# Performance work log

Hardware: AMD Instinct MI355X
Metric: run time of the kernel (lower is better)

Reference implementation:

```python
import jax, jax.numpy as jnp
import numpy as np

DIM = 256
NUM_HEADS = 8


def setup_inputs() -> dict:
    key = jax.random.key(0)
    ks = jax.random.split(key, 8)
    B, H, W = 2, 64, 64
    s = 0.02
    return {
        "query": jax.random.normal(ks[0], (B, H, W, DIM), jnp.float32),
        "sim": jax.random.normal(ks[1], (B, H, W, DIM), jnp.float32),
        "Wq": jax.random.normal(ks[2], (DIM, DIM), jnp.float32) * s,
        "bq": jnp.zeros((DIM,), jnp.float32),
        "Wkv": jax.random.normal(ks[3], (DIM, 2 * DIM), jnp.float32) * s,
        "bkv": jnp.zeros((2 * DIM,), jnp.float32),
        "Wp": jax.random.normal(ks[4], (DIM, DIM), jnp.float32) * s,
        "bp": jnp.zeros((DIM,), jnp.float32),
    }


def reference(query, sim, Wq, bq, Wkv, bkv, Wp, bp):
    B, H, W, dim = query.shape
    nh = NUM_HEADS
    dh = dim // nh
    scale = dh ** (-0.5)
    S = H * W

    # projections
    q = (query.reshape(B, S, dim) @ Wq + bq).reshape(B, S, nh, dh)
    kv = (sim.reshape(B, S, dim) @ Wkv + bkv).reshape(B, S, 2, nh, dh)
    k = kv[:, :, 0]  # [B,S,nh,dh]
    v = kv[:, :, 1]

    # attention: scores [B,nh,S,S]
    attn = jnp.einsum('bqhd,bkhd->bhqk', q * scale, k)
    attn = jax.nn.softmax(attn, axis=-1)
    x = jnp.einsum('bhqk,bkhd->bqhd', attn, v)  # [B,S,nh,dh]
    x = x.reshape(B, H, W, dim)
    return x @ Wp + bp
```

## Files before the change

kernel.cpp:

```cpp
#include <hip/hip_runtime.h>
#include <hip/hip_bf16.h>
#include <math.h>


#define SCALE 0.17677669529663687f
#define LOG2E 1.4426950408889634f

typedef __attribute__((ext_vector_type(8))) short short8;
typedef __attribute__((ext_vector_type(8))) _Float16 half8;
typedef __attribute__((ext_vector_type(4))) float f32x4;

static __device__ __forceinline__ unsigned short f2bf(float x) {
    union { float f; unsigned int u; } v; v.f = x;
    unsigned int r = v.u + 0x7fff + ((v.u >> 16) & 1);
    return (unsigned short)(r >> 16);
}
static __device__ __forceinline__ float bf2f(unsigned short h) {
    union { unsigned int u; float f; } v; v.u = ((unsigned int)h) << 16;
    return v.f;
}
static __device__ __forceinline__ float fexp2(float x) {
#if __has_builtin(__builtin_amdgcn_exp2f)
    return __builtin_amdgcn_exp2f(x);
#else
    float r; asm("v_exp_f32 %0, %1" : "=v"(r) : "v"(x)); return r;
#endif
}
static __device__ __forceinline__ unsigned int pk_bf16(float a, float b) {
    unsigned int r;
    asm("v_cvt_pk_bf16_f32 %0, %1, %2" : "=v"(r) : "v"(a), "v"(b));
    return r;
}
static __device__ __forceinline__ unsigned short f2h(float x) {
    _Float16 h = (_Float16)x;
    union { _Float16 h; unsigned short s; } u; u.h = h;
    return u.s;
}
static __device__ __forceinline__ float h2f(unsigned short s) {
    union { _Float16 h; unsigned short s; } u; u.s = s;
    return (float)u.h;
}

__global__ __launch_bounds__(256) void prep(
    const float* __restrict__ query, const float* __restrict__ sim,
    const float* __restrict__ Wq, const float* __restrict__ Wkv,
    const float* __restrict__ Wp,
    unsigned short* __restrict__ xhi, unsigned short* __restrict__ xlo,
    unsigned short* __restrict__ wfp)
{
    __shared__ float T[64][68];
    const int blk = blockIdx.x, t = threadIdx.x;
    if (blk < 4096) {
        const int e = blk * 1024 + t * 4;
        const float* src = (e < 2097152) ? (query + e) : (sim + (e - 2097152));
        float4 v = *(const float4*)src;
        float xv[4] = {v.x, v.y, v.z, v.w};
        union { unsigned short s[4]; uint2 u; } ph, pl;
#pragma unroll
        for (int j = 0; j < 4; ++j) {
            unsigned short h = f2h(xv[j]);
            ph.s[j] = h;
            pl.s[j] = f2h(xv[j] - h2f(h));
        }
        *(uint2*)&xhi[e] = ph.u;
        *(uint2*)&xlo[e] = pl.u;
        return;
    }
    const int bb = blk - 4096;
    const int mat = bb >> 4, tile = bb & 15;
    const int kr0 = (tile >> 2) * 64;
    const int nc0 = (tile & 3) * 64;
    const float* src; int ldw, cb; float sc = 1.f;
    if (mat == 0)      { src = Wq;  ldw = 256; cb = 0;   sc = SCALE * LOG2E; }
    else if (mat == 1) { src = Wkv; ldw = 512; cb = 0;   }
    else if (mat == 2) { src = Wkv; ldw = 512; cb = 256; }
    else               { src = Wp;  ldw = 256; cb = 0;   }
    {
        const int rl = t >> 4, c4 = (t & 15) * 4;
#pragma unroll
        for (int rr = 0; rr < 4; ++rr) {
            float4 v = *(const float4*)&src[(long long)(kr0 + rr * 16 + rl) * ldw + cb + nc0 + c4];
            T[rr * 16 + rl][c4 + 0] = v.x; T[rr * 16 + rl][c4 + 1] = v.y;
            T[rr * 16 + rl][c4 + 2] = v.z; T[rr * 16 + rl][c4 + 3] = v.w;
        }
    }
    __syncthreads();
    {
        const int nl = t >> 2, kl0 = (t & 3) * 16;
        const long long orow = (long long)(mat * 256 + nc0 + nl) * 256 + kr0 + kl0;
        union { unsigned short s[16]; uint4 u[2]; } ph;
#pragma unroll
        for (int j = 0; j < 16; ++j)
            ph.s[j] = f2h(T[kl0 + j][nl] * sc);
        *(uint4*)&wfp[orow] = ph.u[0];
        *(uint4*)&wfp[orow + 8] = ph.u[1];
    }
}

__global__ __launch_bounds__(256) void gemm_qkv(
    const unsigned short* __restrict__ xhi, const unsigned short* __restrict__ xlo,
    const unsigned short* __restrict__ wfp,
    const float* __restrict__ bq, const float* __restrict__ bkv,
    unsigned short* __restrict__ qbuf, unsigned short* __restrict__ kbuf,
    unsigned short* __restrict__ vTb)
{
    __shared__ unsigned short XsH[64 * 40], XsL[64 * 40], Ws[64 * 40];

    const int t = threadIdx.x, wave = t >> 6, lane = t & 63;
    const int col = lane & 15, quad = lane >> 4;
    const int by = blockIdx.y;
    const int kind = by >> 2;
    const int n0 = (by & 3) * 64;
    const int m0 = blockIdx.x * 64;
    const int xrow0 = ((kind == 0) ? 0 : 8192) + m0;
    const int wrow0 = kind * 256 + n0;
    const int srow = t >> 2, spart = (t & 3) * 8;

    const f32x4 zero = {0.f, 0.f, 0.f, 0.f};
    f32x4 acc[4] = {zero, zero, zero, zero};

    for (int kt = 0; kt < 8; ++kt) {
        const int k0 = kt * 32;
        uint4 xh = *(const uint4*)&xhi[(long long)(xrow0 + srow) * 256 + k0 + spart];
        uint4 xl = *(const uint4*)&xlo[(long long)(xrow0 + srow) * 256 + k0 + spart];
        uint4 wh = *(const uint4*)&wfp[(long long)(wrow0 + srow) * 256 + k0 + spart];
        __syncthreads();
        *(uint4*)&XsH[srow * 40 + spart] = xh;
        *(uint4*)&XsL[srow * 40 + spart] = xl;
        *(uint4*)&Ws[srow * 40 + spart] = wh;
        __syncthreads();

        if (kind < 2) {
            half8 a_h = *(const half8*)(XsH + (wave * 16 + col) * 40 + quad * 8);
            half8 a_l = *(const half8*)(XsL + (wave * 16 + col) * 40 + quad * 8);
#pragma unroll
            for (int nt = 0; nt < 4; ++nt) {
                half8 b = *(const half8*)(Ws + (nt * 16 + col) * 40 + quad * 8);
                acc[nt] = __builtin_amdgcn_mfma_f32_16x16x32_f16(a_h, b, acc[nt], 0, 0, 0);
                acc[nt] = __builtin_amdgcn_mfma_f32_16x16x32_f16(a_l, b, acc[nt], 0, 0, 0);
            }
        } else {
            half8 a = *(const half8*)(Ws + (wave * 16 + col) * 40 + quad * 8);
#pragma unroll
            for (int nt = 0; nt < 4; ++nt) {
                half8 b_h = *(const half8*)(XsH + (nt * 16 + col) * 40 + quad * 8);
                half8 b_l = *(const half8*)(XsL + (nt * 16 + col) * 40 + quad * 8);
                acc[nt] = __builtin_amdgcn_mfma_f32_16x16x32_f16(a, b_h, acc[nt], 0, 0, 0);
                acc[nt] = __builtin_amdgcn_mfma_f32_16x16x32_f16(a, b_l, acc[nt], 0, 0, 0);
            }
        }
    }

    if (kind == 0) {
#pragma unroll
        for (int nt = 0; nt < 4; ++nt) {
            int n = n0 + nt * 16 + col;
            int h = n >> 5, d = n & 31;
            float bias = bq[n] * (SCALE * LOG2E);
#pragma unroll
            for (int r = 0; r < 4; ++r) {
                int mg = m0 + wave * 16 + quad * 4 + r;
                int b = mg >> 12, sidx = mg & 4095;
                qbuf[((long long)(b * 8 + h) * 4096 + sidx) * 32 + d] = f2bf(acc[nt][r] + bias);
            }
        }
    } else if (kind == 1) {
#pragma unroll
        for (int nt = 0; nt < 4; ++nt) {
            int n = n0 + nt * 16 + col;
            int h = n >> 5, d = n & 31;
            float bias = bkv[n];
#pragma unroll
            for (int r = 0; r < 4; ++r) {
                int mg = m0 + wave * 16 + quad * 4 + r;
                int b = mg >> 12, sidx = mg & 4095;
                kbuf[((long long)(b * 8 + h) * 4096 + sidx) * 32 + d] = f2bf(acc[nt][r] + bias);
            }
        }
    } else {
#pragma unroll
        for (int nt = 0; nt < 4; ++nt) {
            int s = m0 + nt * 16 + col;
            int b = s >> 12, sidx = s & 4095;
#pragma unroll
            for (int r = 0; r < 4; ++r) {
                int dcol = n0 + wave * 16 + quad * 4 + r;
                int h = dcol >> 5, dd = dcol & 31;
                float bias = bkv[256 + dcol];
                vTb[((long long)((b * 8 + h) * 32 + dd)) * 4096 + sidx] = f2bf(acc[nt][r] + bias);
            }
        }
    }
}

__global__ __launch_bounds__(256) void flash_mfma(
    const unsigned short* __restrict__ qbuf,
    const unsigned short* __restrict__ kbuf,
    const unsigned short* __restrict__ vT,
    float* __restrict__ xbuf)
{
    __shared__ unsigned short Ks[128 * 40];
    __shared__ unsigned short Vt[32 * 136];
    __shared__ unsigned short Pb[4][640];

    const int t = threadIdx.x;
    const int wave = t >> 6, lane = t & 63;
    const int col = lane & 15, quad = lane >> 4;
    const int bh = blockIdx.x >> 5;
    const int q0 = (blockIdx.x & 31) * 128 + wave * 32;
    const long long kvbase = (long long)bh * 4096 * 32;
    unsigned short* pbw = Pb[wave];

    const short8 qf0 = *(const short8*)(qbuf + kvbase + (long long)(q0 + col) * 32 + quad * 8);
    const short8 qf1 = *(const short8*)(qbuf + kvbase + (long long)(q0 + 16 + col) * 32 + quad * 8);

    const f32x4 zero = {0.f, 0.f, 0.f, 0.f};
    f32x4 o00 = zero, o01 = zero, o10 = zero, o11 = zero;
    float l0 = 0.f, l1 = 0.f;

    const int krow = t >> 2, kpart = (t & 3) * 8;
    const int vrow = t >> 4, vpart = (t & 15) * 8;

    for (int kt = 0; kt < 32; ++kt) {
        uint4 kg0 = *(const uint4*)(kbuf + kvbase + (long long)(kt * 128 + krow) * 32 + kpart);
        uint4 kg1 = *(const uint4*)(kbuf + kvbase + (long long)(kt * 128 + krow + 64) * 32 + kpart);
        uint4 vg0 = *(const uint4*)(vT + ((long long)(bh * 32 + vrow)) * 4096 + kt * 128 + vpart);
        uint4 vg1 = *(const uint4*)(vT + ((long long)(bh * 32 + vrow + 16)) * 4096 + kt * 128 + vpart);
        __syncthreads();
        *(uint4*)(Ks + krow * 40 + kpart) = kg0;
        *(uint4*)(Ks + (krow + 64) * 40 + kpart) = kg1;
        *(uint4*)(Vt + vrow * 136 + vpart) = vg0;
        *(uint4*)(Vt + (vrow + 16) * 136 + vpart) = vg1;
        __syncthreads();

#pragma unroll
        for (int sb = 0; sb < 4; ++sb) {
            const int kb = sb * 32;
            short8 a0 = *(const short8*)(Ks + (kb + col) * 40 + quad * 8);
            short8 a1 = *(const short8*)(Ks + (kb + 16 + col) * 40 + quad * 8);
            short8 v0 = *(const short8*)(Vt + col * 136 + kb + quad * 8);
            short8 v1 = *(const short8*)(Vt + (16 + col) * 136 + kb + quad * 8);
            {
                f32x4 c0 = __builtin_amdgcn_mfma_f32_16x16x32_bf16(a0, qf0, zero, 0, 0, 0);
                f32x4 c1 = __builtin_amdgcn_mfma_f32_16x16x32_bf16(a1, qf0, zero, 0, 0, 0);
                float p0 = fexp2(c0[0]), p1 = fexp2(c0[1]), p2 = fexp2(c0[2]), p3 = fexp2(c0[3]);
                float p4 = fexp2(c1[0]), p5 = fexp2(c1[1]), p6 = fexp2(c1[2]), p7 = fexp2(c1[3]);
                l0 += ((p0 + p1) + (p2 + p3)) + ((p4 + p5) + (p6 + p7));
                uint2 w0 = make_uint2(pk_bf16(p0, p1), pk_bf16(p2, p3));
                uint2 w1 = make_uint2(pk_bf16(p4, p5), pk_bf16(p6, p7));
                *(uint2*)(pbw + col * 40 + quad * 4) = w0;
                *(uint2*)(pbw + col * 40 + 16 + quad * 4) = w1;
                short8 pf = *(const short8*)(pbw + col * 40 + quad * 8);
                o00 = __builtin_amdgcn_mfma_f32_16x16x32_bf16(v0, pf, o00, 0, 0, 0);
                o01 = __builtin_amdgcn_mfma_f32_16x16x32_bf16(v1, pf, o01, 0, 0, 0);
            }
            {
                f32x4 c0 = __builtin_amdgcn_mfma_f32_16x16x32_bf16(a0, qf1, zero, 0, 0, 0);
                f32x4 c1 = __builtin_amdgcn_mfma_f32_16x16x32_bf16(a1, qf1, zero, 0, 0, 0);
                float p0 = fexp2(c0[0]), p1 = fexp2(c0[1]), p2 = fexp2(c0[2]), p3 = fexp2(c0[3]);
                float p4 = fexp2(c1[0]), p5 = fexp2(c1[1]), p6 = fexp2(c1[2]), p7 = fexp2(c1[3]);
                l1 += ((p0 + p1) + (p2 + p3)) + ((p4 + p5) + (p6 + p7));
                uint2 w0 = make_uint2(pk_bf16(p0, p1), pk_bf16(p2, p3));
                uint2 w1 = make_uint2(pk_bf16(p4, p5), pk_bf16(p6, p7));
                *(uint2*)(pbw + col * 40 + quad * 4) = w0;
                *(uint2*)(pbw + col * 40 + 16 + quad * 4) = w1;
                short8 pf = *(const short8*)(pbw + col * 40 + quad * 8);
                o10 = __builtin_amdgcn_mfma_f32_16x16x32_bf16(v0, pf, o10, 0, 0, 0);
                o11 = __builtin_amdgcn_mfma_f32_16x16x32_bf16(v1, pf, o11, 0, 0, 0);
            }
        }
    }

    l0 += __shfl_xor(l0, 16, 64); l0 += __shfl_xor(l0, 32, 64);
    l1 += __shfl_xor(l1, 16, 64); l1 += __shfl_xor(l1, 32, 64);
    const float i0 = 1.f / l0, i1 = 1.f / l1;

    const int b = bh >> 3, hh = bh & 7;
    float* xp0 = xbuf + ((long long)(b * 4096 + q0 + col)) * 256 + hh * 32;
    *(float4*)(xp0 + quad * 4)      = make_float4(o00[0] * i0, o00[1] * i0, o00[2] * i0, o00[3] * i0);
    *(float4*)(xp0 + 16 + quad * 4) = make_float4(o01[0] * i0, o01[1] * i0, o01[2] * i0, o01[3] * i0);
    float* xp1 = xbuf + ((long long)(b * 4096 + q0 + 16 + col)) * 256 + hh * 32;
    *(float4*)(xp1 + quad * 4)      = make_float4(o10[0] * i1, o10[1] * i1, o10[2] * i1, o10[3] * i1);
    *(float4*)(xp1 + 16 + quad * 4) = make_float4(o11[0] * i1, o11[1] * i1, o11[2] * i1, o11[3] * i1);
}

__global__ __launch_bounds__(256) void gemm_outp(
    const float* __restrict__ xbuf, const unsigned short* __restrict__ wfp,
    const float* __restrict__ bp, float* __restrict__ out)
{
    __shared__ unsigned short XsH[64 * 40], XsL[64 * 40], Ws[64 * 40];

    const int t = threadIdx.x, wave = t >> 6, lane = t & 63;
    const int col = lane & 15, quad = lane >> 4;
    const int n0 = blockIdx.y * 64;
    const int m0 = blockIdx.x * 64;
    const int wrow0 = 768 + n0;
    const int srow = t >> 2, spart = (t & 3) * 8;

    const f32x4 zero = {0.f, 0.f, 0.f, 0.f};
    f32x4 acc[4] = {zero, zero, zero, zero};

    for (int kt = 0; kt < 8; ++kt) {
        const int k0 = kt * 32;
        const float* xp = &xbuf[(long long)(m0 + srow) * 256 + k0 + spart];
        float4 xa = *(const float4*)xp;
        float4 xb = *(const float4*)(xp + 4);
        float xv[8] = {xa.x, xa.y, xa.z, xa.w, xb.x, xb.y, xb.z, xb.w};
        union { unsigned short s[8]; uint4 u; } ph, pl;
#pragma unroll
        for (int j = 0; j < 8; ++j) {
            unsigned short h = f2h(xv[j]);
            ph.s[j] = h;
            pl.s[j] = f2h(xv[j] - h2f(h));
        }
        uint4 wh = *(const uint4*)&wfp[(long long)(wrow0 + srow) * 256 + k0 + spart];
        __syncthreads();
        *(uint4*)&XsH[srow * 40 + spart] = ph.u;
        *(uint4*)&XsL[srow * 40 + spart] = pl.u;
        *(uint4*)&Ws[srow * 40 + spart] = wh;
        __syncthreads();

        half8 a_h = *(const half8*)(XsH + (wave * 16 + col) * 40 + quad * 8);
        half8 a_l = *(const half8*)(XsL + (wave * 16 + col) * 40 + quad * 8);
#pragma unroll
        for (int nt = 0; nt < 4; ++nt) {
            half8 b = *(const half8*)(Ws + (nt * 16 + col) * 40 + quad * 8);
            acc[nt] = __builtin_amdgcn_mfma_f32_16x16x32_f16(a_h, b, acc[nt], 0, 0, 0);
            acc[nt] = __builtin_amdgcn_mfma_f32_16x16x32_f16(a_l, b, acc[nt], 0, 0, 0);
        }
    }

#pragma unroll
    for (int nt = 0; nt < 4; ++nt) {
        int n = n0 + nt * 16 + col;
        float bias = bp[n];
#pragma unroll
        for (int r = 0; r < 4; ++r) {
            int mg = m0 + wave * 16 + quad * 4 + r;
            out[(long long)mg * 256 + n] = acc[nt][r] + bias;
        }
    }
}

extern "C" void kernel_launch(void* const* d_in, const int* in_sizes, int n_in,
                              void* d_out, int out_size, void* d_ws, size_t ws_size,
                              hipStream_t stream) {
    const float* query = (const float*)d_in[0];
    const float* sim   = (const float*)d_in[1];
    const float* Wq    = (const float*)d_in[2];
    const float* bq    = (const float*)d_in[3];
    const float* Wkv   = (const float*)d_in[4];
    const float* bkv   = (const float*)d_in[5];
    const float* Wp    = (const float*)d_in[6];
    const float* bp    = (const float*)d_in[7];
    float* out = (float*)d_out;

    unsigned short* wsb = (unsigned short*)d_ws;
    unsigned short* qbuf = wsb;
    unsigned short* kbuf = wsb + 2097152;
    unsigned short* vT   = wsb + 4194304;
    unsigned short* wfp  = wsb + 6291456;
    unsigned short* xhi  = wsb + 6553600;
    unsigned short* xlo  = wsb + 10747904;
    float* xbuf = (float*)(wsb + 6553600);

    prep      <<<dim3(4160),    256, 0, stream>>>(query, sim, Wq, Wkv, Wp,
                                                  xhi, xlo, wfp);
    gemm_qkv  <<<dim3(128, 12), 256, 0, stream>>>(xhi, xlo, wfp, bq, bkv,
                                                  qbuf, kbuf, vT);
    flash_mfma<<<dim3(512),     256, 0, stream>>>(qbuf, kbuf, vT, xbuf);
    gemm_outp <<<dim3(128, 4),  256, 0, stream>>>(xbuf, wfp, bp, out);
}
```

Baseline: 172.6 us.

## Split attention KV range in two and raise queries per wave to four tiles

Each wave of the flash kernel now handles 64 queries instead of 32, so every K/V tile staged in shared memory feeds twice as much work. The key sequence is split into two halves across blocks to keep the grid size at 512. Each half writes unnormalized partial outputs and row sums, and the output projection combines the halves and normalizes them while loading. In exchange, the flash kernel uses more registers and shared memory, and the partial outputs double the traffic into the final GEMM. Dropping the running max relies on the score range being small, which the code before already assumed.

```diff
diff --git a/kernel.cpp b/kernel.cpp
--- a/kernel.cpp
+++ b/kernel.cpp
@@ -197,31 +197,35 @@
     const unsigned short* __restrict__ qbuf,
     const unsigned short* __restrict__ kbuf,
     const unsigned short* __restrict__ vT,
-    float* __restrict__ xbuf)
+    float* __restrict__ xpart, float* __restrict__ lpart)
 {
     __shared__ unsigned short Ks[128 * 40];
     __shared__ unsigned short Vt[32 * 136];
-    __shared__ unsigned short Pb[4][640];
+    __shared__ unsigned short Pb[16][640];
 
     const int t = threadIdx.x;
     const int wave = t >> 6, lane = t & 63;
     const int col = lane & 15, quad = lane >> 4;
-    const int bh = blockIdx.x >> 5;
-    const int q0 = (blockIdx.x & 31) * 128 + wave * 32;
+    const int qb = blockIdx.x & 15;
+    const int bh = (blockIdx.x >> 4) & 15;
+    const int ks = blockIdx.x >> 8;
+    const int q0 = qb * 256 + wave * 64;
     const long long kvbase = (long long)bh * 4096 * 32;
-    unsigned short* pbw = Pb[wave];
-
-    const short8 qf0 = *(const short8*)(qbuf + kvbase + (long long)(q0 + col) * 32 + quad * 8);
-    const short8 qf1 = *(const short8*)(qbuf + kvbase + (long long)(q0 + 16 + col) * 32 + quad * 8);
+
+    short8 qf[4];
+#pragma unroll
+    for (int i = 0; i < 4; ++i)
+        qf[i] = *(const short8*)(qbuf + kvbase + (long long)(q0 + i * 16 + col) * 32 + quad * 8);
 
     const f32x4 zero = {0.f, 0.f, 0.f, 0.f};
-    f32x4 o00 = zero, o01 = zero, o10 = zero, o11 = zero;
-    float l0 = 0.f, l1 = 0.f;
+    f32x4 o[8] = {zero, zero, zero, zero, zero, zero, zero, zero};
+    float l[4] = {0.f, 0.f, 0.f, 0.f};
 
     const int krow = t >> 2, kpart = (t & 3) * 8;
     const int vrow = t >> 4, vpart = (t & 15) * 8;
 
-    for (int kt = 0; kt < 32; ++kt) {
+    for (int kt0 = 0; kt0 < 16; ++kt0) {
+        const int kt = ks * 16 + kt0;
         uint4 kg0 = *(const uint4*)(kbuf + kvbase + (long long)(kt * 128 + krow) * 32 + kpart);
         uint4 kg1 = *(const uint4*)(kbuf + kvbase + (long long)(kt * 128 + krow + 64) * 32 + kpart);
         uint4 vg0 = *(const uint4*)(vT + ((long long)(bh * 32 + vrow)) * 4096 + kt * 128 + vpart);
@@ -240,52 +244,49 @@
             short8 a1 = *(const short8*)(Ks + (kb + 16 + col) * 40 + quad * 8);
             short8 v0 = *(const short8*)(Vt + col * 136 + kb + quad * 8);
             short8 v1 = *(const short8*)(Vt + (16 + col) * 136 + kb + quad * 8);
-            {
-                f32x4 c0 = __builtin_amdgcn_mfma_f32_16x16x32_bf16(a0, qf0, zero, 0, 0, 0);
-                f32x4 c1 = __builtin_amdgcn_mfma_f32_16x16x32_bf16(a1, qf0, zero, 0, 0, 0);
+#pragma unroll
+            for (int i = 0; i < 4; ++i) {
+                f32x4 c0 = __builtin_amdgcn_mfma_f32_16x16x32_bf16(a0, qf[i], zero, 0, 0, 0);
+                f32x4 c1 = __builtin_amdgcn_mfma_f32_16x16x32_bf16(a1, qf[i], zero, 0, 0, 0);
                 float p0 = fexp2(c0[0]), p1 = fexp2(c0[1]), p2 = fexp2(c0[2]), p3 = fexp2(c0[3]);
                 float p4 = fexp2(c1[0]), p5 = fexp2(c1[1]), p6 = fexp2(c1[2]), p7 = fexp2(c1[3]);
-                l0 += ((p0 + p1) + (p2 + p3)) + ((p4 + p5) + (p6 + p7));
+                l[i] += ((p0 + p1) + (p2 + p3)) + ((p4 + p5) + (p6 + p7));
                 uint2 w0 = make_uint2(pk_bf16(p0, p1), pk_bf16(p2, p3));
                 uint2 w1 = make_uint2(pk_bf16(p4, p5), pk_bf16(p6, p7));
+                unsigned short* pbw = Pb[wave * 4 + i];
                 *(uint2*)(pbw + col * 40 + quad * 4) = w0;
                 *(uint2*)(pbw + col * 40 + 16 + quad * 4) = w1;
                 short8 pf = *(const short8*)(pbw + col * 40 + quad * 8);
-                o00 = __builtin_amdgcn_mfma_f32_16x16x32_bf16(v0, pf, o00, 0, 0, 0);
-                o01 = __builtin_amdgcn_mfma_f32_16x16x32_bf16(v1, pf, o01, 0, 0, 0);
-            }
-            {
-                f32x4 c0 = __builtin_amdgcn_mfma_f32_16x16x32_bf16(a0, qf1, zero, 0, 0, 0);
-                f32x4 c1 = __builtin_amdgcn_mfma_f32_16x16x32_bf16(a1, qf1, zero, 0, 0, 0);
-                float p0 = fexp2(c0[0]), p1 = fexp2(c0[1]), p2 = fexp2(c0[2]), p3 = fexp2(c0[3]);
-                float p4 = fexp2(c1[0]), p5 = fexp2(c1[1]), p6 = fexp2(c1[2]), p7 = fexp2(c1[3]);
-                l1 += ((p0 + p1) + (p2 + p3)) + ((p4 + p5) + (p6 + p7));
-                uint2 w0 = make_uint2(pk_bf16(p0, p1), pk_bf16(p2, p3));
-                uint2 w1 = make_uint2(pk_bf16(p4, p5), pk_bf16(p6, p7));
-                *(uint2*)(pbw + col * 40 + quad * 4) = w0;
-                *(uint2*)(pbw + col * 40 + 16 + quad * 4) = w1;
-                short8 pf = *(const short8*)(pbw + col * 40 + quad * 8);
-                o10 = __builtin_amdgcn_mfma_f32_16x16x32_bf16(v0, pf, o10, 0, 0, 0);
-                o11 = __builtin_amdgcn_mfma_f32_16x16x32_bf16(v1, pf, o11, 0, 0, 0);
-            }
-        }
-    }
-
-    l0 += __shfl_xor(l0, 16, 64); l0 += __shfl_xor(l0, 32, 64);
-    l1 += __shfl_xor(l1, 16, 64); l1 += __shfl_xor(l1, 32, 64);
-    const float i0 = 1.f / l0, i1 = 1.f / l1;
+                o[2 * i]     = __builtin_amdgcn_mfma_f32_16x16x32_bf16(v0, pf, o[2 * i], 0, 0, 0);
+                o[2 * i + 1] = __builtin_amdgcn_mfma_f32_16x16x32_bf16(v1, pf, o[2 * i + 1], 0, 0, 0);
+            }
+        }
+    }
+
+#pragma unroll
+    for (int i = 0; i < 4; ++i) {
+        l[i] += __shfl_xor(l[i], 16, 64);
+        l[i] += __shfl_xor(l[i], 32, 64);
+    }
 
     const int b = bh >> 3, hh = bh & 7;
-    float* xp0 = xbuf + ((long long)(b * 4096 + q0 + col)) * 256 + hh * 32;
-    *(float4*)(xp0 + quad * 4)      = make_float4(o00[0] * i0, o00[1] * i0, o00[2] * i0, o00[3] * i0);
-    *(float4*)(xp0 + 16 + quad * 4) = make_float4(o01[0] * i0, o01[1] * i0, o01[2] * i0, o01[3] * i0);
-    float* xp1 = xbuf + ((long long)(b * 4096 + q0 + 16 + col)) * 256 + hh * 32;
-    *(float4*)(xp1 + quad * 4)      = make_float4(o10[0] * i1, o10[1] * i1, o10[2] * i1, o10[3] * i1);
-    *(float4*)(xp1 + 16 + quad * 4) = make_float4(o11[0] * i1, o11[1] * i1, o11[2] * i1, o11[3] * i1);
+    float* xp = xpart + (long long)ks * 2097152;
+#pragma unroll
+    for (int i = 0; i < 4; ++i) {
+        float* row = xp + ((long long)(b * 4096 + q0 + i * 16 + col)) * 256 + hh * 32;
+        *(float4*)(row + quad * 4)      = make_float4(o[2*i][0], o[2*i][1], o[2*i][2], o[2*i][3]);
+        *(float4*)(row + 16 + quad * 4) = make_float4(o[2*i+1][0], o[2*i+1][1], o[2*i+1][2], o[2*i+1][3]);
+    }
+    float lv = l[0];
+    if (quad == 1) lv = l[1];
+    else if (quad == 2) lv = l[2];
+    else if (quad == 3) lv = l[3];
+    lpart[ks * 65536 + bh * 4096 + q0 + quad * 16 + col] = lv;
 }
 
 __global__ __launch_bounds__(256) void gemm_outp(
-    const float* __restrict__ xbuf, const unsigned short* __restrict__ wfp,
+    const float* __restrict__ xpart, const float* __restrict__ lpart,
+    const unsigned short* __restrict__ wfp,
     const float* __restrict__ bp, float* __restrict__ out)
 {
     __shared__ unsigned short XsH[64 * 40], XsL[64 * 40], Ws[64 * 40];
@@ -296,22 +297,34 @@
     const int m0 = blockIdx.x * 64;
     const int wrow0 = 768 + n0;
     const int srow = t >> 2, spart = (t & 3) * 8;
+    const int r = m0 + srow;
+    const int bidx = r >> 12, s = r & 4095;
+    const float* __restrict__ xa = xpart;
+    const float* __restrict__ xb = xpart + 2097152;
 
     const f32x4 zero = {0.f, 0.f, 0.f, 0.f};
     f32x4 acc[4] = {zero, zero, zero, zero};
 
     for (int kt = 0; kt < 8; ++kt) {
         const int k0 = kt * 32;
-        const float* xp = &xbuf[(long long)(m0 + srow) * 256 + k0 + spart];
-        float4 xa = *(const float4*)xp;
-        float4 xb = *(const float4*)(xp + 4);
-        float xv[8] = {xa.x, xa.y, xa.z, xa.w, xb.x, xb.y, xb.z, xb.w};
-        union { unsigned short s[8]; uint4 u; } ph, pl;
+        const int head = k0 >> 5;
+        float la = lpart[(bidx * 8 + head) * 4096 + s];
+        float lb = lpart[65536 + (bidx * 8 + head) * 4096 + s];
+        float linv = 1.f / (la + lb);
+        const float* pa = &xa[(long long)r * 256 + k0 + spart];
+        const float* pb = &xb[(long long)r * 256 + k0 + spart];
+        float4 a0 = *(const float4*)pa, a1 = *(const float4*)(pa + 4);
+        float4 b0 = *(const float4*)pb, b1 = *(const float4*)(pb + 4);
+        float xv[8] = {(a0.x + b0.x) * linv, (a0.y + b0.y) * linv,
+                       (a0.z + b0.z) * linv, (a0.w + b0.w) * linv,
+                       (a1.x + b1.x) * linv, (a1.y + b1.y) * linv,
+                       (a1.z + b1.z) * linv, (a1.w + b1.w) * linv};
+        union { unsigned short s4[8]; uint4 u; } ph, pl;
 #pragma unroll
         for (int j = 0; j < 8; ++j) {
             unsigned short h = f2h(xv[j]);
-            ph.s[j] = h;
-            pl.s[j] = f2h(xv[j] - h2f(h));
+            ph.s4[j] = h;
+            pl.s4[j] = f2h(xv[j] - h2f(h));
         }
         uint4 wh = *(const uint4*)&wfp[(long long)(wrow0 + srow) * 256 + k0 + spart];
         __syncthreads();
@@ -335,9 +348,9 @@
         int n = n0 + nt * 16 + col;
         float bias = bp[n];
 #pragma unroll
-        for (int r = 0; r < 4; ++r) {
-            int mg = m0 + wave * 16 + quad * 4 + r;
-            out[(long long)mg * 256 + n] = acc[nt][r] + bias;
+        for (int rr = 0; rr < 4; ++rr) {
+            int mg = m0 + wave * 16 + quad * 4 + rr;
+            out[(long long)mg * 256 + n] = acc[nt][rr] + bias;
         }
     }
 }
@@ -362,12 +375,13 @@
     unsigned short* wfp  = wsb + 6291456;
     unsigned short* xhi  = wsb + 6553600;
     unsigned short* xlo  = wsb + 10747904;
-    float* xbuf = (float*)(wsb + 6553600);
+    float* xpart = (float*)(wsb + 6553600);
+    float* lpart = (float*)(wsb + 14942208);
 
     prep      <<<dim3(4160),    256, 0, stream>>>(query, sim, Wq, Wkv, Wp,
                                                   xhi, xlo, wfp);
     gemm_qkv  <<<dim3(128, 12), 256, 0, stream>>>(xhi, xlo, wfp, bq, bkv,
                                                   qbuf, kbuf, vT);
-    flash_mfma<<<dim3(512),     256, 0, stream>>>(qbuf, kbuf, vT, xbuf);
-    gemm_outp <<<dim3(128, 4),  256, 0, stream>>>(xbuf, wfp, bp, out);
-}
+    flash_mfma<<<dim3(512),     256, 0, stream>>>(qbuf, kbuf, vT, xpart, lpart);
+    gemm_outp <<<dim3(128, 4),  256, 0, stream>>>(xpart, lpart, wfp, bp, out);
+}
```

Result: no change. 170.3 us (-1.3%).
